# Kernel optimization log

Measured on AMD Instinct MI355X. Metric: run time of the kernel, lower is better.

Reference implementation:

```python
import jax, jax.numpy as jnp
import numpy as np

DIM = 1024
HEADS = 16
HEAD_DIM = DIM // HEADS
B, N = 4, 4096


def setup_inputs() -> dict:
    key = jax.random.key(0)
    k1, k2, k3, k4, k5 = jax.random.split(key, 5)
    scale_in = 1.0 / np.sqrt(DIM)
    return {
        "x": jax.random.normal(k1, (B, N, DIM), dtype=jnp.float32),
        # torch nn.Linear convention: weight [out, in], y = x @ W.T + b
        "w_qkv": jax.random.uniform(k2, (3 * DIM, DIM), jnp.float32, -scale_in, scale_in),
        "b_qkv": jax.random.uniform(k3, (3 * DIM,), jnp.float32, -scale_in, scale_in),
        "w_proj": jax.random.uniform(k4, (DIM, DIM), jnp.float32, -scale_in, scale_in),
        "b_proj": jax.random.uniform(k5, (DIM,), jnp.float32, -scale_in, scale_in),
    }


def reference(x, w_qkv, b_qkv, w_proj, b_proj):
    Bx, Nx, C = x.shape
    H, D = HEADS, HEAD_DIM
    qkv = (x @ w_qkv.T + b_qkv).reshape(Bx, Nx, 3, H, D)
    q, k, v = qkv[:, :, 0], qkv[:, :, 1], qkv[:, :, 2]  # each [B, N, H, D]
    # NOTE: faithful to source — heads dim was NOT moved to batch position,
    # so attention mixes across heads per token: scores [B, N, H, H].
    scores = jnp.einsum('bnhd,bngd->bnhg', q, k) / jnp.sqrt(jnp.asarray(D, x.dtype))
    attn = jax.nn.softmax(scores, axis=-1)
    out = jnp.einsum('bnhg,bngd->bnhd', attn, v).reshape(Bx, Nx, C)
    return out @ w_proj.T + b_proj
```

## Files before the change

### kernel.cpp

```cpp
#include <hip/hip_runtime.h>
#include <hip/hip_bf16.h>
#include <stdint.h>

typedef __bf16 v8bf __attribute__((ext_vector_type(8)));
typedef float  v4f  __attribute__((ext_vector_type(4)));
typedef unsigned short u16;

#define NTOK 16384
#define KDIM 1024

__device__ __forceinline__ u16 f2bf(float f) {
  uint32_t b = __builtin_bit_cast(uint32_t, f);
  b += 0x7FFFu + ((b >> 16) & 1u);
  return (u16)(b >> 16);
}

__device__ __forceinline__ void gl_lds16(const u16* g, u16* l) {
  __builtin_amdgcn_global_load_lds(
      (const __attribute__((address_space(1))) uint32_t*)g,
      (__attribute__((address_space(3))) uint32_t*)l,
      16, 0, 0);
}

__device__ __forceinline__ void bar() {
  __builtin_amdgcn_sched_barrier(0);
  __builtin_amdgcn_s_barrier();
  __builtin_amdgcn_sched_barrier(0);
}
#define LGKM0() do { asm volatile("s_waitcnt lgkmcnt(0)" ::: "memory"); \
                     __builtin_amdgcn_sched_barrier(0); } while (0)
#define VMW(n)  do { asm volatile("s_waitcnt vmcnt(" #n ")" ::: "memory"); \
                     __builtin_amdgcn_sched_barrier(0); } while (0)

__global__ void cvt_all(const float* __restrict__ x, const float* __restrict__ wq,
                        const float* __restrict__ wp, u16* __restrict__ xo,
                        u16* __restrict__ wqo, u16* __restrict__ wpo) {
  size_t id = (size_t)blockIdx.x * 256 + threadIdx.x;
  const float* src; u16* dst;
  if (id < 2097152)      { src = x  + id * 8;              dst = xo  + id * 8; }
  else if (id < 2490368) { src = wq + (id - 2097152) * 8;  dst = wqo + (id - 2097152) * 8; }
  else                   { src = wp + (id - 2490368) * 8;  dst = wpo + (id - 2490368) * 8; }
  float4 a = *(const float4*)(src);
  float4 b = *(const float4*)(src + 4);
  union { u16 u[8]; uint4 v; } pk;
  pk.u[0]=f2bf(a.x); pk.u[1]=f2bf(a.y); pk.u[2]=f2bf(a.z); pk.u[3]=f2bf(a.w);
  pk.u[4]=f2bf(b.x); pk.u[5]=f2bf(b.y); pk.u[6]=f2bf(b.z); pk.u[7]=f2bf(b.w);
  *(uint4*)(dst) = pk.v;
}

template<int NTOT, bool OUT_BF16>
__global__ __launch_bounds__(512, 2)
void gemm_bt(const u16* __restrict__ A, const u16* __restrict__ Bw,
             const float* __restrict__ bias, void* __restrict__ out) {
  constexpr int NM = NTOK / 256;
  constexpr int NN = NTOT / 256;
  constexpr int NWG = NM * NN;
  constexpr int NT = KDIM / 64;
  const int bid = blockIdx.x;
  const int swz = (bid & 7) * (NWG / 8) + (bid >> 3);
  const int bm = swz % NM, bn = swz / NM;

  extern __shared__ __align__(16) u16 smem[];

  const int tid = threadIdx.x, lane = tid & 63, w = tid >> 6;
  const int wr = w >> 2, wc = w & 3;

  v4f acc[8][4];
#pragma unroll
  for (int i = 0; i < 8; ++i)
#pragma unroll
    for (int j = 0; j < 4; ++j) acc[i][j] = v4f{0.f, 0.f, 0.f, 0.f};

  const u16* Ab = A  + (size_t)bm * 256 * KDIM;
  const u16* Bb = Bw + (size_t)bn * 256 * KDIM;

  const int srow = tid >> 3;
  const int sc   = (tid & 7) ^ (srow & 7);
  const size_t soff = (size_t)srow * KDIM + (size_t)sc * 8;
  auto stageH = [&](int dstoff, const u16* src) {
    gl_lds16(src + soff, smem + dstoff + (size_t)tid * 8);
    gl_lds16(src + soff + (size_t)64 * KDIM, smem + dstoff + (size_t)tid * 8 + 4096);
  };

  const int rA  = lane & 15;
  const int ck0 = (((lane >> 4) ^ (lane & 7)) << 3);
  const int ck1 = ((((lane >> 4) + 4) ^ (lane & 7)) << 3);
  const int ha = wr * 8192;
  const int hb = 16384 + (wc >> 1) * 8192 + (wc & 1) * 64 * 64;

  v8bf Af[4][2], B0[2][2], B1[2][2];

#define MM16(FI, GI, BF) do {                                                 \
  _Pragma("unroll") for (int f = 0; f < 4; ++f)                               \
  _Pragma("unroll") for (int g = 0; g < 2; ++g) {                             \
    acc[(FI)+f][(GI)+g] = __builtin_amdgcn_mfma_f32_16x16x32_bf16(            \
        Af[f][0], BF[g][0], acc[(FI)+f][(GI)+g], 0, 0, 0);                    \
    acc[(FI)+f][(GI)+g] = __builtin_amdgcn_mfma_f32_16x16x32_bf16(            \
        Af[f][1], BF[g][1], acc[(FI)+f][(GI)+g], 0, 0, 0);                    \
  }                                                                           \
} while (0)

#define TILE(T, D, DN, ST, VM) do {                                           \
                                                            \
  _Pragma("unroll") for (int f = 0; f < 4; ++f) {                             \
    Af[f][0] = *(const v8bf*)(smem + (D) + ha + (f*16 + rA)*64 + ck0);        \
    Af[f][1] = *(const v8bf*)(smem + (D) + ha + (f*16 + rA)*64 + ck1); }      \
  _Pragma("unroll") for (int g = 0; g < 2; ++g) {                             \
    B0[g][0] = *(const v8bf*)(smem + (D) + hb + (g*16 + rA)*64 + ck0);        \
    B0[g][1] = *(const v8bf*)(smem + (D) + hb + (g*16 + rA)*64 + ck1); }      \
  if (ST) stageH((DN) + 8192, Ab + (size_t)128*KDIM + (size_t)((T)+1)*64);    \
  bar(); LGKM0();                                                             \
  __builtin_amdgcn_s_setprio(1); MM16(0, 0, B0);                              \
  __builtin_amdgcn_s_setprio(0); bar();                                       \
                                                            \
  _Pragma("unroll") for (int g = 0; g < 2; ++g) {                             \
    B1[g][0] = *(const v8bf*)(smem + (D) + hb + (32 + g*16 + rA)*64 + ck0);   \
    B1[g][1] = *(const v8bf*)(smem + (D) + hb + (32 + g*16 + rA)*64 + ck1); } \
  if (ST) stageH((DN) + 16384, Bb + (size_t)((T)+1)*64);                      \
  bar(); LGKM0();                                                             \
  __builtin_amdgcn_s_setprio(1); MM16(0, 2, B1);                              \
  __builtin_amdgcn_s_setprio(0); bar();                                       \
                                                            \
  _Pragma("unroll") for (int f = 0; f < 4; ++f) {                             \
    Af[f][0] = *(const v8bf*)(smem + (D) + ha + (64 + f*16 + rA)*64 + ck0);   \
    Af[f][1] = *(const v8bf*)(smem + (D) + ha + (64 + f*16 + rA)*64 + ck1); } \
  if (ST) stageH((DN) + 24576, Bb + (size_t)128*KDIM + (size_t)((T)+1)*64);   \
  bar(); LGKM0();                                                             \
  __builtin_amdgcn_s_setprio(1); MM16(4, 2, B1);                              \
  __builtin_amdgcn_s_setprio(0); bar();                                       \
                                                            \
  if ((VM) == 2) stageH((D) + 0, Ab + (size_t)((T)+2)*64);                    \
  bar();                                                                      \
  __builtin_amdgcn_s_setprio(1); MM16(4, 0, B0);                              \
  __builtin_amdgcn_s_setprio(0);                                              \
  if ((VM) == 2) { VMW(2); } else if ((VM) == 0) { VMW(0); }                  \
  bar();                                                                      \
} while (0)

  stageH(0,     Ab);
  stageH(8192,  Ab + (size_t)128 * KDIM);
  stageH(16384, Bb);
  stageH(24576, Bb + (size_t)128 * KDIM);
  stageH(32768, Ab + 64);
  VMW(2);
  bar();

  for (int j = 0; j < 7; ++j) {
    const int t0 = 2 * j;
    TILE(t0,     0,     32768, 1, 2);
    TILE(t0 + 1, 32768, 0,     1, 2);
  }
  TILE(14, 0,     32768, 1, 0);
  TILE(15, 32768, 0,     0, -1);
#undef TILE
#undef MM16

  const int col0 = bn * 256 + wc * 64 + (lane & 15);
  const int row0 = bm * 256 + wr * 128 + ((lane >> 4) << 2);
#pragma unroll
  for (int mf = 0; mf < 8; ++mf) {
#pragma unroll
    for (int nf = 0; nf < 4; ++nf) {
      const int gc = col0 + nf * 16;
      const float bv = bias[gc];
#pragma unroll
      for (int j = 0; j < 4; ++j) {
        const size_t idx = (size_t)(row0 + mf * 16 + j) * NTOT + gc;
        const float v = acc[mf][nf][j] + bv;
        if constexpr (OUT_BF16) ((u16*)out)[idx] = f2bf(v);
        else                    ((float*)out)[idx] = v;
      }
    }
  }
}

__global__ __launch_bounds__(256)
void attn_mix(const u16* __restrict__ qkv, u16* __restrict__ outp) {
  __shared__ __align__(16) u16 sq[4][3072];
  __shared__ float sp[4][16][16];
  const int tid = threadIdx.x, lane = tid & 63, w = tid >> 6;
  const size_t tok = (size_t)blockIdx.x * 4 + w;
  const u16* src = qkv + tok * 3072;
#pragma unroll
  for (int i = 0; i < 6; ++i) {
    int t = i * 64 + lane;
    int row = t >> 3;
    int c = (t & 7) ^ (row & 7);
    gl_lds16(src + row * 64 + c * 8, &sq[w][t * 8]);
  }
  __syncthreads();

  const int h = lane >> 2, gb = lane & 3;
  v8bf qv[8];
#pragma unroll
  for (int c = 0; c < 8; ++c)
    qv[c] = *(const v8bf*)&sq[w][h * 64 + ((c ^ (h & 7)) * 8)];

  float s[4];
#pragma unroll
  for (int g4 = 0; g4 < 4; ++g4) {
    const int g = gb * 4 + g4;
    float a = 0.f;
#pragma unroll
    for (int c = 0; c < 8; ++c) {
      v8bf kv = *(const v8bf*)&sq[w][1024 + g * 64 + ((c ^ (g & 7)) * 8)];
#pragma unroll
      for (int j = 0; j < 8; ++j) a += (float)qv[c][j] * (float)kv[j];
    }
    s[g4] = a * 0.125f;
  }
  float m = fmaxf(fmaxf(s[0], s[1]), fmaxf(s[2], s[3]));
  m = fmaxf(m, __shfl_xor(m, 1));
  m = fmaxf(m, __shfl_xor(m, 2));
  float p[4], sum = 0.f;
#pragma unroll
  for (int g4 = 0; g4 < 4; ++g4) { p[g4] = __expf(s[g4] - m); sum += p[g4]; }
  sum += __shfl_xor(sum, 1);
  sum += __shfl_xor(sum, 2);
  const float inv = 1.f / sum;
#pragma unroll
  for (int g4 = 0; g4 < 4; ++g4) sp[w][h][gb * 4 + g4] = p[g4] * inv;
  __syncthreads();

  float o[16];
#pragma unroll
  for (int j = 0; j < 16; ++j) o[j] = 0.f;
  const int db = gb;
#pragma unroll
  for (int g = 0; g < 16; ++g) {
    const float a = sp[w][h][g];
    v8bf v0 = *(const v8bf*)&sq[w][2048 + g * 64 + (((db * 2)     ^ (g & 7)) * 8)];
    v8bf v1 = *(const v8bf*)&sq[w][2048 + g * 64 + (((db * 2 + 1) ^ (g & 7)) * 8)];
#pragma unroll
    for (int j = 0; j < 8; ++j) { o[j] += a * (float)v0[j]; o[8 + j] += a * (float)v1[j]; }
  }
  union { u16 u[16]; uint4 v[2]; } ob;
#pragma unroll
  for (int j = 0; j < 16; ++j) ob.u[j] = f2bf(o[j]);
  u16* dst = outp + tok * 1024 + h * 64 + db * 16;
  *(uint4*)dst = ob.v[0];
  *((uint4*)dst + 1) = ob.v[1];
}

extern "C" void kernel_launch(void* const* d_in, const int* in_sizes, int n_in,
                              void* d_out, int out_size, void* d_ws, size_t ws_size,
                              hipStream_t stream) {
  const float* x      = (const float*)d_in[0];
  const float* w_qkv  = (const float*)d_in[1];
  const float* b_qkv  = (const float*)d_in[2];
  const float* w_proj = (const float*)d_in[3];
  const float* b_proj = (const float*)d_in[4];

  char* ws = (char*)d_ws;
  u16* x_bf    = (u16*)(ws);
  u16* wqkv_bf = (u16*)(ws + (size_t)33554432);
  u16* wp_bf   = (u16*)(ws + (size_t)39845888);
  u16* qkv_bf  = (u16*)(ws + (size_t)41943040);
  u16* at_bf   = (u16*)(ws + (size_t)142606336);

  (void)hipFuncSetAttribute((const void*)&gemm_bt<3072, true>,
                            hipFuncAttributeMaxDynamicSharedMemorySize, 131072);
  (void)hipFuncSetAttribute((const void*)&gemm_bt<1024, false>,
                            hipFuncAttributeMaxDynamicSharedMemorySize, 131072);

  cvt_all<<<dim3(10240), dim3(256), 0, stream>>>(x, w_qkv, w_proj,
                                                 x_bf, wqkv_bf, wp_bf);

  gemm_bt<3072, true ><<<dim3(768), dim3(512), 131072, stream>>>(x_bf, wqkv_bf, b_qkv, qkv_bf);
  attn_mix<<<dim3(4096), dim3(256), 0, stream>>>(qkv_bf, at_bf);
  gemm_bt<1024, false><<<dim3(256), dim3(512), 131072, stream>>>(at_bf, wp_bf, b_proj, d_out);
}
```

Before: 216.4 us.

## Restructure GEMM main loop to prefetch next tile's LDS fragments during MFMA

Reworks the double-buffered bf16 GEMM K-loop so the whole next K-tile is staged two steps ahead. Register fragments for the following tile are read from LDS while the current MFMAs run, instead of at the start of each phase. The prologue now stages two full tiles and preloads the first A/B fragments. The aim is to hide LDS read latency and cut barrier stalls between MFMA groups, at the cost of deeper global-load outstanding counts and more register pressure from holding the prefetched fragments.

```diff
diff --git a/kernel.cpp b/kernel.cpp
--- a/kernel.cpp
+++ b/kernel.cpp
@@ -55,7 +55,6 @@
   constexpr int NM = NTOK / 256;
   constexpr int NN = NTOT / 256;
   constexpr int NWG = NM * NN;
-  constexpr int NT = KDIM / 64;
   const int bid = blockIdx.x;
   const int swz = (bid & 7) * (NWG / 8) + (bid >> 3);
   const int bm = swz % NM, bn = swz / NM;
@@ -88,9 +87,20 @@
   const int ha = wr * 8192;
   const int hb = 16384 + (wc >> 1) * 8192 + (wc & 1) * 64 * 64;
 
-  v8bf Af[4][2], B0[2][2], B1[2][2];
-
+  v8bf Af[4][2], B0r[2][2], B1r[2][2];
+
+#define RD_A(BUF, ROFF) do {                                                  \
+  _Pragma("unroll") for (int f = 0; f < 4; ++f) {                             \
+    Af[f][0] = *(const v8bf*)(smem + (BUF) + ha + ((ROFF)+f*16+rA)*64 + ck0); \
+    Af[f][1] = *(const v8bf*)(smem + (BUF) + ha + ((ROFF)+f*16+rA)*64 + ck1);}\
+} while (0)
+#define RD_B(BUF, REG, ROFF) do {                                             \
+  _Pragma("unroll") for (int g = 0; g < 2; ++g) {                             \
+    REG[g][0] = *(const v8bf*)(smem + (BUF) + hb + ((ROFF)+g*16+rA)*64 + ck0);\
+    REG[g][1] = *(const v8bf*)(smem + (BUF) + hb + ((ROFF)+g*16+rA)*64 + ck1);}\
+} while (0)
 #define MM16(FI, GI, BF) do {                                                 \
+  __builtin_amdgcn_s_setprio(1);                                              \
   _Pragma("unroll") for (int f = 0; f < 4; ++f)                               \
   _Pragma("unroll") for (int g = 0; g < 2; ++g) {                             \
     acc[(FI)+f][(GI)+g] = __builtin_amdgcn_mfma_f32_16x16x32_bf16(            \
@@ -98,42 +108,28 @@
     acc[(FI)+f][(GI)+g] = __builtin_amdgcn_mfma_f32_16x16x32_bf16(            \
         Af[f][1], BF[g][1], acc[(FI)+f][(GI)+g], 0, 0, 0);                    \
   }                                                                           \
-} while (0)
-
-#define TILE(T, D, DN, ST, VM) do {                                           \
-                                                            \
-  _Pragma("unroll") for (int f = 0; f < 4; ++f) {                             \
-    Af[f][0] = *(const v8bf*)(smem + (D) + ha + (f*16 + rA)*64 + ck0);        \
-    Af[f][1] = *(const v8bf*)(smem + (D) + ha + (f*16 + rA)*64 + ck1); }      \
-  _Pragma("unroll") for (int g = 0; g < 2; ++g) {                             \
-    B0[g][0] = *(const v8bf*)(smem + (D) + hb + (g*16 + rA)*64 + ck0);        \
-    B0[g][1] = *(const v8bf*)(smem + (D) + hb + (g*16 + rA)*64 + ck1); }      \
-  if (ST) stageH((DN) + 8192, Ab + (size_t)128*KDIM + (size_t)((T)+1)*64);    \
-  bar(); LGKM0();                                                             \
-  __builtin_amdgcn_s_setprio(1); MM16(0, 0, B0);                              \
-  __builtin_amdgcn_s_setprio(0); bar();                                       \
-                                                            \
-  _Pragma("unroll") for (int g = 0; g < 2; ++g) {                             \
-    B1[g][0] = *(const v8bf*)(smem + (D) + hb + (32 + g*16 + rA)*64 + ck0);   \
-    B1[g][1] = *(const v8bf*)(smem + (D) + hb + (32 + g*16 + rA)*64 + ck1); } \
-  if (ST) stageH((DN) + 16384, Bb + (size_t)((T)+1)*64);                      \
-  bar(); LGKM0();                                                             \
-  __builtin_amdgcn_s_setprio(1); MM16(0, 2, B1);                              \
-  __builtin_amdgcn_s_setprio(0); bar();                                       \
-                                                            \
-  _Pragma("unroll") for (int f = 0; f < 4; ++f) {                             \
-    Af[f][0] = *(const v8bf*)(smem + (D) + ha + (64 + f*16 + rA)*64 + ck0);   \
-    Af[f][1] = *(const v8bf*)(smem + (D) + ha + (64 + f*16 + rA)*64 + ck1); } \
-  if (ST) stageH((DN) + 24576, Bb + (size_t)128*KDIM + (size_t)((T)+1)*64);   \
-  bar(); LGKM0();                                                             \
-  __builtin_amdgcn_s_setprio(1); MM16(4, 2, B1);                              \
-  __builtin_amdgcn_s_setprio(0); bar();                                       \
-                                                            \
-  if ((VM) == 2) stageH((D) + 0, Ab + (size_t)((T)+2)*64);                    \
+  __builtin_amdgcn_s_setprio(0);                                              \
+} while (0)
+
+#define TILE(T, D, DN, ST, PR) do {                                           \
+                                                                      \
+  LGKM0(); MM16(0, 0, B0r); bar();                                            \
+                                                                      \
+  VMW(0);                                                                     \
+  if (ST) stageH((D) + 16384, Bb + (size_t)((T)+2) * 64);                     \
+  LGKM0(); MM16(0, 2, B1r);                                                   \
+  RD_A((D), 64);                                                              \
   bar();                                                                      \
-  __builtin_amdgcn_s_setprio(1); MM16(4, 0, B0);                              \
-  __builtin_amdgcn_s_setprio(0);                                              \
-  if ((VM) == 2) { VMW(2); } else if ((VM) == 0) { VMW(0); }                  \
+                                                                      \
+  if (ST) stageH((D) + 24576, Bb + (size_t)128*KDIM + (size_t)((T)+2) * 64);  \
+  LGKM0(); MM16(4, 2, B1r);                                                   \
+  if (PR) RD_B((DN), B1r, 32);                                                \
+  bar();                                                                      \
+                                                                      \
+  if (ST) { stageH((D) + 0,    Ab + (size_t)((T)+2) * 64);                    \
+            stageH((D) + 8192, Ab + (size_t)128*KDIM + (size_t)((T)+2)*64); } \
+  LGKM0(); MM16(4, 0, B0r);                                                   \
+  if (PR) { RD_A((DN), 0); RD_B((DN), B0r, 0); }                              \
   bar();                                                                      \
 } while (0)
 
@@ -141,19 +137,26 @@
   stageH(8192,  Ab + (size_t)128 * KDIM);
   stageH(16384, Bb);
   stageH(24576, Bb + (size_t)128 * KDIM);
-  stageH(32768, Ab + 64);
-  VMW(2);
+  stageH(32768 + 16384, Bb + 64);
+  stageH(32768 + 24576, Bb + (size_t)128 * KDIM + 64);
+  stageH(32768 + 0,     Ab + 64);
+  stageH(32768 + 8192,  Ab + (size_t)128 * KDIM + 64);
+  VMW(8);
   bar();
+  RD_A(0, 0);
+  RD_B(0, B0r, 0);
+  RD_B(0, B1r, 32);
 
   for (int j = 0; j < 7; ++j) {
-    const int t0 = 2 * j;
-    TILE(t0,     0,     32768, 1, 2);
-    TILE(t0 + 1, 32768, 0,     1, 2);
-  }
-  TILE(14, 0,     32768, 1, 0);
-  TILE(15, 32768, 0,     0, -1);
+    TILE(2 * j,     0,     32768, 1, 1);
+    TILE(2 * j + 1, 32768, 0,     1, 1);
+  }
+  TILE(14, 0,     32768, 0, 1);
+  TILE(15, 32768, 0,     0, 0);
 #undef TILE
 #undef MM16
+#undef RD_A
+#undef RD_B
 
   const int col0 = bn * 256 + wc * 64 + (lane & 15);
   const int row0 = bm * 256 + wr * 128 + ((lane >> 4) << 2);
```

New measurement: 206.8 us. -4.4%, faster.
